# Optimization experiments

Hardware: AMD Instinct MI355X
Metric: run time of the kernel (lower is better)

## Reference

```python
import jax, jax.numpy as jnp
import numpy as np

N_NODES = 50000
N_EDGES = 800000
HID = 128
DEPTH = 10
N_GRAPHS = 512
IN_F = 32


def setup_inputs() -> dict:
    key = jax.random.key(0)
    ks = jax.random.split(key, 12)
    x = jax.random.normal(ks[0], (N_NODES, IN_F), jnp.float32)
    edge_index = jax.random.randint(ks[1], (2, N_EDGES), 0, N_NODES, dtype=jnp.int32)
    batch_map = jnp.sort(jax.random.randint(ks[2], (N_NODES,), 0, N_GRAPHS, dtype=jnp.int32))
    # parameters (PyG GraphConv: lin_rel has bias, lin_root has no bias)
    W_embed = jax.random.normal(ks[3], (IN_F, HID), jnp.float32) * 0.1
    W_rel = jax.random.normal(ks[4], (DEPTH, HID, HID), jnp.float32) * 0.05
    b_rel = jax.random.normal(ks[5], (DEPTH, HID), jnp.float32) * 0.01
    W_root = jax.random.normal(ks[6], (DEPTH, HID, HID), jnp.float32) * 0.05
    W_ws = jax.random.normal(ks[7], (DEPTH * HID, 1), jnp.float32) * 0.05
    b_ws = jax.random.normal(ks[8], (1,), jnp.float32) * 0.01
    W_sg = jax.random.normal(ks[9], (DEPTH * HID, IN_F), jnp.float32) * 0.05
    b_sg = jax.random.normal(ks[10], (IN_F,), jnp.float32) * 0.01
    return {
        "x": x, "edge_index": edge_index, "batch_map": batch_map,
        "num_graphs": N_GRAPHS,
        "W_embed": W_embed, "W_rel": W_rel, "b_rel": b_rel, "W_root": W_root,
        "W_ws": W_ws, "b_ws": b_ws, "W_sg": W_sg, "b_sg": b_sg,
    }


def reference(x, edge_index, batch_map, num_graphs,
              W_embed, W_rel, b_rel, W_root, W_ws, b_ws, W_sg, b_sg):
    n = x.shape[0]
    src, dst = edge_index[0], edge_index[1]
    h = x @ W_embed  # [N, 128]
    reps = []
    for i in range(DEPTH):
        # PyG GraphConv (aggr='add'): lin_rel(sum_j h_j) + lin_root(h_i)
        agg = jax.ops.segment_sum(h[src], dst, num_segments=n)  # [N, 128]
        h = agg @ W_rel[i] + b_rel[i] + h @ W_root[i]
        reps.append(h)
    out = jnp.concatenate(reps, axis=1)  # [N, 1280]
    # softmax over last dim of [N,1] logits (faithful: yields ones)
    sum_w = jax.nn.softmax(out @ W_ws + b_ws, axis=-1)  # [N, 1]
    out = sum_w * out
    pooled = jax.ops.segment_sum(out, batch_map, num_segments=num_graphs)  # [G, 1280]
    return pooled @ W_sg + b_sg  # [G, 32]
```

## Files before the change

### kernel.cpp

```cpp
#include <hip/hip_runtime.h>

#define N_NODES 50000
#define N_EDGES 800000
#define HID 128
#define DEPTH 10
#define N_GRAPHS 512
#define IN_F 32

#define BM 128
#define GBLK (50048 / BM)
#define PADN 50048

#define ROWW 256

#define SB 256
#define NSB ((N_NODES + SB - 1) / SB)

#define KSTEPS 24
#define PACK_CHUNKS (DEPTH * KSTEPS * 512)

typedef __attribute__((ext_vector_type(8))) short short8;
typedef __attribute__((ext_vector_type(4))) float f32x4;
typedef __attribute__((ext_vector_type(4))) unsigned uint4v;

__device__ __forceinline__ float bf2f(short u) {
    union { unsigned i; float f; } v; v.i = ((unsigned)(unsigned short)u) << 16; return v.f;
}
__device__ __forceinline__ short f2bf(float f) {
    union { float f; unsigned i; } v; v.f = f;
    unsigned r = (v.i + 0x7FFFu + ((v.i >> 16) & 1u)) >> 16;
    return (short)r;
}
__device__ __forceinline__ unsigned pack2(short lo, short hi) {
    return ((unsigned)(unsigned short)hi << 16) | (unsigned)(unsigned short)lo;
}

__global__ __launch_bounds__(256) void pack_weights(
    const float* __restrict__ Wrel, const float* __restrict__ Wroot,
    short* __restrict__ Bp) {
    int idx = blockIdx.x * 256 + threadIdx.x;
    if (idx >= PACK_CHUNKS) return;
    int layer = idx / (KSTEPS * 512);
    int rem = idx - layer * KSTEPS * 512;
    int ks = rem >> 9;
    int c = rem & 511;
    int kslot = c >> 7, n = c & 127;
    int term = ks >> 2;
    int kc = (ks & 3) * 32;
    const float* W = (term < 3 ? Wrel : Wroot) + (size_t)layer * HID * HID;
    bool lo = (term == 1 || term == 4);
    short out[8];
#pragma unroll
    for (int j = 0; j < 8; ++j) {
        int k = kc + kslot * 8 + j;
        float v = W[(size_t)k * HID + n];
        short hi = f2bf(v);
        if (lo) { v = v - bf2f(hi); hi = f2bf(v); }
        out[j] = hi;
    }
    *reinterpret_cast<short8*>(Bp + (size_t)idx * 8) = *reinterpret_cast<short8*>(out);
}

__global__ __launch_bounds__(128) void embed_kernel(
    const float* __restrict__ x, const float* __restrict__ W,
    short* __restrict__ hIL, short* __restrict__ hHr) {
    __shared__ float Ws[IN_F * HID];
    int t = threadIdx.x;
    for (int i = t; i < IN_F * HID; i += 128) Ws[i] = W[i];
    __syncthreads();
    int nbeg = blockIdx.x * 50;
    for (int n = nbeg; n < nbeg + 50; ++n) {
        float acc = 0.f;
#pragma unroll
        for (int k = 0; k < IN_F; ++k)
            acc += x[(size_t)n * IN_F + k] * Ws[k * HID + t];
        short hh = f2bf(acc);
        hIL[(size_t)n * ROWW + t] = hh;
        hIL[(size_t)n * ROWW + HID + t] = f2bf(acc - bf2f(hh));
        hHr[(size_t)n * HID + t] = hh;
    }
}

__global__ __launch_bounds__(256) void hist_kernel(const int* __restrict__ idx, int* __restrict__ count, int n) {
    int e = blockIdx.x * 256 + threadIdx.x;
    if (e < n) atomicAdd(&count[idx[e]], 1);
}

__global__ __launch_bounds__(SB) void scan_part1(
    const int* __restrict__ count, int* __restrict__ bsum, int n) {
    __shared__ int s[SB];
    int t = threadIdx.x;
    int i = blockIdx.x * SB + t;
    s[t] = (i < n) ? count[i] : 0;
    __syncthreads();
    for (int off = SB / 2; off >= 1; off >>= 1) {
        if (t < off) s[t] += s[t + off];
        __syncthreads();
    }
    if (t == 0) bsum[blockIdx.x] = s[0];
}

__global__ __launch_bounds__(256) void scan_part2(
    const int* __restrict__ bsum, int* __restrict__ boff, int nb) {
    __shared__ int s[256];
    int t = threadIdx.x;
    int v0 = (t < nb) ? bsum[t] : 0;
    s[t] = v0;
    __syncthreads();
    for (int off = 1; off < 256; off <<= 1) {
        int v = (t >= off) ? s[t - off] : 0;
        __syncthreads();
        s[t] += v;
        __syncthreads();
    }
    boff[t] = (t == 0) ? 0 : s[t - 1];
}

__global__ __launch_bounds__(SB) void scan_part3(
    const int* __restrict__ count, const int* __restrict__ boff,
    int* __restrict__ ptr, int* __restrict__ cursor, int n) {
    __shared__ int s[SB];
    int b = blockIdx.x, t = threadIdx.x;
    int i = b * SB + t;
    int v = (i < n) ? count[i] : 0;
    s[t] = v;
    __syncthreads();
    for (int off = 1; off < SB; off <<= 1) {
        int u = (t >= off) ? s[t - off] : 0;
        __syncthreads();
        s[t] += u;
        __syncthreads();
    }
    int excl = s[t] - v + boff[b];
    if (i < n) {
        ptr[i] = excl;
        cursor[i] = excl;
        if (i == n - 1) ptr[n] = excl + v;
    }
}

__global__ __launch_bounds__(256) void scatter_kernel(
    const int* __restrict__ src, const int* __restrict__ dst,
    int* __restrict__ cursor, int* __restrict__ sorted_src) {
    int e = blockIdx.x * 256 + threadIdx.x;
    if (e < N_EDGES) {
        int p = atomicAdd(&cursor[dst[e]], 1);
        sorted_src[p] = src[e];
    }
}

__global__ __launch_bounds__(256) void aggregate_kernel(
    const short* __restrict__ hHr, const int* __restrict__ row_ptr,
    const int* __restrict__ sorted_src, short* __restrict__ agg2) {
    int n = (blockIdx.x * 256 + threadIdx.x) >> 6;
    int lane = threadIdx.x & 63;
    const unsigned* __restrict__ R = (const unsigned*)hHr;
    int beg = row_ptr[n], end = row_ptr[n + 1];
    float a0 = 0.f, a1 = 0.f;
#define ACC(v) do { \
        union { unsigned u; float f; } u0, u1; \
        u0.u = (v) << 16; u1.u = (v) & 0xFFFF0000u; \
        a0 += u0.f; a1 += u1.f; } while (0)
    int j = beg;
    for (; j + 8 <= end; j += 8) {
        unsigned v[8];
#pragma unroll
        for (int u = 0; u < 8; ++u) {
            int s = __builtin_amdgcn_readfirstlane(sorted_src[j + u]);
            v[u] = R[(size_t)s * 64 + lane];
        }
#pragma unroll
        for (int u = 0; u < 8; ++u) ACC(v[u]);
    }
    for (; j + 2 <= end; j += 2) {
        int s0 = __builtin_amdgcn_readfirstlane(sorted_src[j]);
        int s1 = __builtin_amdgcn_readfirstlane(sorted_src[j + 1]);
        unsigned v0 = R[(size_t)s0 * 64 + lane];
        unsigned v1 = R[(size_t)s1 * 64 + lane];
        ACC(v0); ACC(v1);
    }
    if (j < end) {
        int s = __builtin_amdgcn_readfirstlane(sorted_src[j]);
        unsigned v = R[(size_t)s * 64 + lane];
        ACC(v);
    }
#undef ACC
    short h0 = f2bf(a0), h1 = f2bf(a1);
    unsigned hw = pack2(h0, h1);
    unsigned lw = pack2(f2bf(a0 - bf2f(h0)), f2bf(a1 - bf2f(h1)));
    ((unsigned*)agg2)[(size_t)n * 128 + lane] = hw;
    ((unsigned*)agg2)[(size_t)n * 128 + 64 + lane] = lw;
}

__global__ __launch_bounds__(512) void layer_gemm_mfma(
    const short* __restrict__ agg2, const short* __restrict__ hIL,
    const short* __restrict__ Bp, const float* __restrict__ bias,
    short* __restrict__ outIL, short* __restrict__ outH,
    const int* __restrict__ bmap, float* __restrict__ pooled, int layer,
    int write_h) {
    __shared__ __align__(16) char smem[34304];
    short* AbBuf = (short*)smem;
    short* BbBuf = (short*)(smem + 16384);
    float* Cs    = (float*)smem;
    int*   bmapS = (int*)(smem + 33792);

    int tid = threadIdx.x;
    int lane = tid & 63;
    int w = tid >> 6;
    int wr = w >> 2, wc = w & 3;
    int m0 = blockIdx.x * BM;

    int r0 = tid >> 2, q0 = tid & 3;

    f32x4 acc[4][2];
#pragma unroll
    for (int m = 0; m < 4; ++m)
#pragma unroll
        for (int n = 0; n < 2; ++n) acc[m][n] = (f32x4)0.f;

#define A_ADDR(src, row, f0, plane) \
    ((src) + (size_t)(row) * ROWW + (plane) * HID + (f0))

    {
        short8 a0 = *reinterpret_cast<const short8*>(A_ADDR(agg2, m0 + r0, q0 * 8, 0));
        short8 b0 = *reinterpret_cast<const short8*>(Bp + (size_t)tid * 8);
        *reinterpret_cast<short8*>(&AbBuf[(q0 * 128 + r0) * 8]) = a0;
        *reinterpret_cast<short8*>(&BbBuf[tid * 8]) = b0;
    }
    __syncthreads();

    int kb = lane >> 4;
    int rr = lane & 15;

    for (int ks = 0; ks < KSTEPS; ++ks) {
        int cur = ks & 1;
        short8 a0, b0;
        if (ks < KSTEPS - 1) {
            int nks = ks + 1;
            int term = nks >> 2;
            int kc = (nks & 3) * 32;
            const short* src2 = (term <= 2) ? agg2 : hIL;
            int plane = (term == 2 || term == 5) ? 1 : 0;
            a0 = *reinterpret_cast<const short8*>(A_ADDR(src2, m0 + r0, kc + q0 * 8, plane));
            b0 = *reinterpret_cast<const short8*>(Bp + (size_t)nks * 4096 + (size_t)tid * 8);
        }
        short8 af[4], bfr[2];
#pragma unroll
        for (int m = 0; m < 4; ++m)
            af[m] = *reinterpret_cast<const short8*>(&AbBuf[cur * 4096 + (kb * 128 + wr * 64 + m * 16 + rr) * 8]);
#pragma unroll
        for (int n = 0; n < 2; ++n)
            bfr[n] = *reinterpret_cast<const short8*>(&BbBuf[cur * 4096 + (kb * 128 + wc * 32 + n * 16 + rr) * 8]);
#pragma unroll
        for (int m = 0; m < 4; ++m)
#pragma unroll
            for (int n = 0; n < 2; ++n)
                acc[m][n] = __builtin_amdgcn_mfma_f32_16x16x32_bf16(af[m], bfr[n], acc[m][n], 0, 0, 0);
        if (ks < KSTEPS - 1) {
            int nb = cur ^ 1;
            *reinterpret_cast<short8*>(&AbBuf[nb * 4096 + (q0 * 128 + r0) * 8]) = a0;
            *reinterpret_cast<short8*>(&BbBuf[nb * 4096 + tid * 8]) = b0;
        }
        __syncthreads();
    }
#undef A_ADDR

    if (tid < 128) {
        int gi = m0 + tid;
        bmapS[tid] = bmap[gi < N_NODES ? gi : N_NODES - 1];
    }
    float bs[2];
    {
        int col = wc * 32 + rr;
#pragma unroll
        for (int n = 0; n < 2; ++n) bs[n] = bias[col + n * 16];
    }
    int colP = tid & 127;
    int quarter = tid >> 7;

    for (int c = 0; c < 2; ++c) {
        if (wr == c) {
            int colb = wc * 32 + rr;
#pragma unroll
            for (int m = 0; m < 4; ++m) {
#pragma unroll
                for (int n = 0; n < 2; ++n) {
#pragma unroll
                    for (int i = 0; i < 4; ++i) {
                        int lr = m * 16 + kb * 4 + i;
                        Cs[lr * 132 + colb + n * 16] = acc[m][n][i] + bs[n];
                    }
                }
            }
        }
        __syncthreads();

        if (write_h) {
#pragma unroll
            for (int pq = 0; pq < 2; ++pq) {
                int idx = pq * 512 + tid;
                int lr = idx >> 4;
                int oct = idx & 15;
                const float4* crow = reinterpret_cast<const float4*>(&Cs[lr * 132 + oct * 8]);
                float4 c0 = crow[0], c1 = crow[1];
                float v[8] = {c0.x, c0.y, c0.z, c0.w, c1.x, c1.y, c1.z, c1.w};
                unsigned hw[4], lw[4];
#pragma unroll
                for (int k = 0; k < 4; ++k) {
                    short ha = f2bf(v[2 * k]), hb = f2bf(v[2 * k + 1]);
                    short la = f2bf(v[2 * k] - bf2f(ha)), lb = f2bf(v[2 * k + 1] - bf2f(hb));
                    hw[k] = pack2(ha, hb);
                    lw[k] = pack2(la, lb);
                }
                int row = m0 + c * 64 + lr;
                unsigned* oI = (unsigned*)(outIL + (size_t)row * ROWW);
                unsigned* oH = (unsigned*)(outH + (size_t)row * HID);
                uint4v hv; hv.x = hw[0]; hv.y = hw[1]; hv.z = hw[2]; hv.w = hw[3];
                uint4v lv; lv.x = lw[0]; lv.y = lw[1]; lv.z = lw[2]; lv.w = lw[3];
                *reinterpret_cast<uint4v*>(oI + oct * 4) = hv;
                *reinterpret_cast<uint4v*>(oI + 64 + oct * 4) = lv;
                *reinterpret_cast<uint4v*>(oH + oct * 4) = hv;
            }
        }

        {
            float pacc = 0.f;
            int gprev = -1;
            float* pbase = pooled + (size_t)layer * HID + colP;
            for (int q = 0; q < 16; ++q) {
                int lr = quarter * 16 + q;
                int grow = m0 + c * 64 + lr;
                if (grow >= N_NODES) break;
                int g = bmapS[c * 64 + lr];
                float v = Cs[lr * 132 + colP];
                if (g != gprev) {
                    if (gprev >= 0) atomicAdd(pbase + (size_t)gprev * (DEPTH * HID), pacc);
                    gprev = g; pacc = v;
                } else {
                    pacc += v;
                }
            }
            if (gprev >= 0) atomicAdd(pbase + (size_t)gprev * (DEPTH * HID), pacc);
        }
        __syncthreads();
    }
}

__global__ __launch_bounds__(256) void final_kernel(
    const float* __restrict__ pooled, const float* __restrict__ Wsg,
    const float* __restrict__ bsg, float* __restrict__ out) {
    int t = threadIdx.x & 31;
    int g = blockIdx.x * 8 + (threadIdx.x >> 5);
    float acc = bsg[t];
    const float* prow = pooled + (size_t)g * (DEPTH * HID);
    for (int k = 0; k < DEPTH * HID; ++k)
        acc += prow[k] * Wsg[k * IN_F + t];
    out[g * IN_F + t] = acc;
}

extern "C" void kernel_launch(void* const* d_in, const int* in_sizes, int n_in,
                              void* d_out, int out_size, void* d_ws, size_t ws_size,
                              hipStream_t stream) {
    const float* x       = (const float*)d_in[0];
    const int*   edge    = (const int*)d_in[1];
    const int*   bmap    = (const int*)d_in[2];
    const float* W_embed = (const float*)d_in[4];
    const float* W_rel   = (const float*)d_in[5];
    const float* b_rel   = (const float*)d_in[6];
    const float* W_root  = (const float*)d_in[7];
    const float* W_sg    = (const float*)d_in[10];
    const float* b_sg    = (const float*)d_in[11];
    float* out = (float*)d_out;

    const int* src = edge;
    const int* dst = edge + N_EDGES;

    char* ws = (char*)d_ws;
    auto alloc = [&](size_t bytes) -> char* {
        char* p = ws;
        ws += (bytes + 255) & ~(size_t)255;
        return p;
    };
    const size_t rowB = (size_t)PADN * ROWW * 2;
    const size_t hB   = (size_t)PADN * HID * 2;
    short* h_a   = (short*)alloc(rowB);
    short* h_b   = (short*)alloc(rowB);
    short* hHr   = (short*)alloc(hB);
    short* agg2  = (short*)alloc(rowB);
    float* pooled = (float*)alloc((size_t)N_GRAPHS * DEPTH * HID * 4);
    int* counts     = (int*)alloc((size_t)N_NODES * 4);
    int* row_ptr    = (int*)alloc((size_t)(N_NODES + 1) * 4);
    int* cursor     = (int*)alloc((size_t)N_NODES * 4);
    int* sorted_src = (int*)alloc((size_t)N_EDGES * 4);
    int* bsum       = (int*)alloc((size_t)256 * 4);
    int* boff       = (int*)alloc((size_t)256 * 4);
    short* Bpacked  = (short*)alloc((size_t)PACK_CHUNKS * 8 * 2);

    hipMemsetAsync(counts, 0, (size_t)N_NODES * 4, stream);
    hipMemsetAsync(pooled, 0, (size_t)N_GRAPHS * DEPTH * HID * 4, stream);

    pack_weights<<<(PACK_CHUNKS + 255) / 256, 256, 0, stream>>>(W_rel, W_root, Bpacked);
    embed_kernel<<<1000, 128, 0, stream>>>(x, W_embed, h_a, hHr);

    hist_kernel<<<(N_EDGES + 255) / 256, 256, 0, stream>>>(dst, counts, N_EDGES);
    scan_part1<<<NSB, SB, 0, stream>>>(counts, bsum, N_NODES);
    scan_part2<<<1, 256, 0, stream>>>(bsum, boff, NSB);
    scan_part3<<<NSB, SB, 0, stream>>>(counts, boff, row_ptr, cursor, N_NODES);
    scatter_kernel<<<(N_EDGES + 255) / 256, 256, 0, stream>>>(src, dst, cursor, sorted_src);

    short *hc = h_a, *hn = h_b;
    for (int i = 0; i < DEPTH; ++i) {
        aggregate_kernel<<<(N_NODES + 3) / 4, 256, 0, stream>>>(hHr, row_ptr, sorted_src, agg2);
        layer_gemm_mfma<<<GBLK, 512, 0, stream>>>(agg2, hc,
                                                  Bpacked + (size_t)i * KSTEPS * 4096,
                                                  b_rel + (size_t)i * HID,
                                                  hn, hHr, bmap, pooled, i,
                                                  (i < DEPTH - 1) ? 1 : 0);
        short* t = hc; hc = hn; hn = t;
    }

    final_kernel<<<N_GRAPHS / 8, 256, 0, stream>>>(pooled, W_sg, b_sg, out);
}
```

Measured before the change: 802.7 us.

## Restructure GEMM k-loop to reuse A tiles; privatize histogram and bin CSR scatter

The layer GEMM now loads each A tile (agg hi/lo plane, h hi/lo plane) once and multiplies it by one or two packed B tiles (hi and lo weight splits), giving 16 A stages instead of 24. This cuts A-tile global loads and barriers per block. It costs more shared memory for a double-width B buffer. Separately, the edge histogram writes into 8 privatized count planes that are summed in the scan, and the CSR scatter bins destinations into 8 node ranges per edge chunk to reduce atomic contention and improve locality, at the cost of each edge being read 8 times.

New measurement: 716.1 us. -10.8%, faster.

```diff
diff --git a/kernel.cpp b/kernel.cpp
--- a/kernel.cpp
+++ b/kernel.cpp
@@ -16,8 +16,14 @@
 #define SB 256
 #define NSB ((N_NODES + SB - 1) / SB)
 
-#define KSTEPS 24
-#define PACK_CHUNKS (DEPTH * KSTEPS * 512)
+#define NBIN 8
+#define BINW ((N_NODES + NBIN - 1) / NBIN)
+#define NCH 125
+#define CHSZ (N_EDGES / NCH)
+
+#define NBT 24
+#define NAST 16
+#define PACK_CHUNKS (DEPTH * NBT * 512)
 
 typedef __attribute__((ext_vector_type(8))) short short8;
 typedef __attribute__((ext_vector_type(4))) float f32x4;
@@ -40,19 +46,22 @@
     short* __restrict__ Bp) {
     int idx = blockIdx.x * 256 + threadIdx.x;
     if (idx >= PACK_CHUNKS) return;
-    int layer = idx / (KSTEPS * 512);
-    int rem = idx - layer * KSTEPS * 512;
-    int ks = rem >> 9;
+    int layer = idx / (NBT * 512);
+    int rem = idx - layer * NBT * 512;
+    int t = rem >> 9;
     int c = rem & 511;
     int kslot = c >> 7, n = c & 127;
-    int term = ks >> 2;
-    int kc = (ks & 3) * 32;
-    const float* W = (term < 3 ? Wrel : Wroot) + (size_t)layer * HID * HID;
-    bool lo = (term == 1 || term == 4);
+    int kc, lo;
+    const float* W;
+    if (t < 8)       { kc = t >> 1;        W = Wrel;  lo = t & 1; }
+    else if (t < 12) { kc = t - 8;         W = Wrel;  lo = 0; }
+    else if (t < 20) { kc = (t - 12) >> 1; W = Wroot; lo = t & 1; }
+    else             { kc = t - 20;        W = Wroot; lo = 0; }
+    W += (size_t)layer * HID * HID;
     short out[8];
 #pragma unroll
     for (int j = 0; j < 8; ++j) {
-        int k = kc + kslot * 8 + j;
+        int k = kc * 32 + kslot * 8 + j;
         float v = W[(size_t)k * HID + n];
         short hi = f2bf(v);
         if (lo) { v = v - bf2f(hi); hi = f2bf(v); }
@@ -81,17 +90,26 @@
     }
 }
 
-__global__ __launch_bounds__(256) void hist_kernel(const int* __restrict__ idx, int* __restrict__ count, int n) {
+__global__ __launch_bounds__(256) void hist8_kernel(
+    const int* __restrict__ dst, int* __restrict__ counts8) {
     int e = blockIdx.x * 256 + threadIdx.x;
-    if (e < n) atomicAdd(&count[idx[e]], 1);
+    int plane = blockIdx.x & 7;
+    if (e < N_EDGES) atomicAdd(&counts8[(size_t)plane * N_NODES + dst[e]], 1);
 }
 
 __global__ __launch_bounds__(SB) void scan_part1(
-    const int* __restrict__ count, int* __restrict__ bsum, int n) {
+    const int* __restrict__ counts8, int* __restrict__ counts,
+    int* __restrict__ bsum, int n) {
     __shared__ int s[SB];
     int t = threadIdx.x;
     int i = blockIdx.x * SB + t;
-    s[t] = (i < n) ? count[i] : 0;
+    int v = 0;
+    if (i < n) {
+#pragma unroll
+        for (int p = 0; p < 8; ++p) v += counts8[(size_t)p * N_NODES + i];
+        counts[i] = v;
+    }
+    s[t] = v;
     __syncthreads();
     for (int off = SB / 2; off >= 1; off >>= 1) {
         if (t < off) s[t] += s[t + off];
@@ -139,13 +157,21 @@
     }
 }
 
-__global__ __launch_bounds__(256) void scatter_kernel(
+__global__ __launch_bounds__(256) void scatter8_kernel(
     const int* __restrict__ src, const int* __restrict__ dst,
     int* __restrict__ cursor, int* __restrict__ sorted_src) {
-    int e = blockIdx.x * 256 + threadIdx.x;
-    if (e < N_EDGES) {
-        int p = atomicAdd(&cursor[dst[e]], 1);
-        sorted_src[p] = src[e];
+    int s = blockIdx.x & 7;
+    int c = blockIdx.x >> 3;
+    int lo = s * BINW;
+    int hi = lo + BINW;
+    int base = c * CHSZ;
+    for (int e = base + threadIdx.x; e < base + CHSZ; e += 256) {
+        int d = dst[e];
+        int sv = src[e];
+        if (d >= lo && d < hi) {
+            int p = atomicAdd(&cursor[d], 1);
+            sorted_src[p] = sv;
+        }
     }
 }
 
@@ -198,11 +224,11 @@
     short* __restrict__ outIL, short* __restrict__ outH,
     const int* __restrict__ bmap, float* __restrict__ pooled, int layer,
     int write_h) {
-    __shared__ __align__(16) char smem[34304];
+    __shared__ __align__(16) char smem[49664];
     short* AbBuf = (short*)smem;
     short* BbBuf = (short*)(smem + 16384);
     float* Cs    = (float*)smem;
-    int*   bmapS = (int*)(smem + 33792);
+    int*   bmapS = (int*)(smem + 49152);
 
     int tid = threadIdx.x;
     int lane = tid & 63;
@@ -218,52 +244,73 @@
 #pragma unroll
         for (int n = 0; n < 2; ++n) acc[m][n] = (f32x4)0.f;
 
-#define A_ADDR(src, row, f0, plane) \
-    ((src) + (size_t)(row) * ROWW + (plane) * HID + (f0))
+#define NB_OF(a)   ((((a) >> 2) & 1) ? 1 : 2)
+#define BOFF_OF(a) (((a) < 4) ? (a) * 2 : ((a) < 8) ? 8 + ((a) - 4) \
+                    : ((a) < 12) ? 12 + ((a) - 8) * 2 : 20 + ((a) - 12))
+#define A_PTR(a) ((((a) >> 2) <= 1 ? agg2 : hIL) + ((((a) >> 2) & 1) ? HID : 0))
 
     {
-        short8 a0 = *reinterpret_cast<const short8*>(A_ADDR(agg2, m0 + r0, q0 * 8, 0));
+        const short* Ap = A_PTR(0);
+        short8 a0 = *reinterpret_cast<const short8*>(Ap + (size_t)(m0 + r0) * ROWW + q0 * 8);
         short8 b0 = *reinterpret_cast<const short8*>(Bp + (size_t)tid * 8);
+        short8 b1 = *reinterpret_cast<const short8*>(Bp + 4096 * 8 / 8 * 8 + (size_t)tid * 8 + 4096);
+        b1 = *reinterpret_cast<const short8*>(Bp + (size_t)4096 + (size_t)tid * 8);
         *reinterpret_cast<short8*>(&AbBuf[(q0 * 128 + r0) * 8]) = a0;
         *reinterpret_cast<short8*>(&BbBuf[tid * 8]) = b0;
+        *reinterpret_cast<short8*>(&BbBuf[4096 + tid * 8]) = b1;
     }
     __syncthreads();
 
     int kb = lane >> 4;
     int rr = lane & 15;
 
-    for (int ks = 0; ks < KSTEPS; ++ks) {
-        int cur = ks & 1;
-        short8 a0, b0;
-        if (ks < KSTEPS - 1) {
-            int nks = ks + 1;
-            int term = nks >> 2;
-            int kc = (nks & 3) * 32;
-            const short* src2 = (term <= 2) ? agg2 : hIL;
-            int plane = (term == 2 || term == 5) ? 1 : 0;
-            a0 = *reinterpret_cast<const short8*>(A_ADDR(src2, m0 + r0, kc + q0 * 8, plane));
-            b0 = *reinterpret_cast<const short8*>(Bp + (size_t)nks * 4096 + (size_t)tid * 8);
-        }
-        short8 af[4], bfr[2];
+    for (int a = 0; a < NAST; ++a) {
+        int cur = a & 1;
+        int nb = NB_OF(a);
+        short8 an, bn0, bn1;
+        int nbn = 0;
+        if (a < NAST - 1) {
+            int na = a + 1;
+            nbn = NB_OF(na);
+            int kc = (na & 3) * 32;
+            const short* Ap = A_PTR(na) + kc;
+            an = *reinterpret_cast<const short8*>(Ap + (size_t)(m0 + r0) * ROWW + q0 * 8);
+            const short* Bsrc = Bp + (size_t)BOFF_OF(na) * 4096;
+            bn0 = *reinterpret_cast<const short8*>(Bsrc + (size_t)tid * 8);
+            if (nbn == 2)
+                bn1 = *reinterpret_cast<const short8*>(Bsrc + (size_t)4096 + (size_t)tid * 8);
+        }
+        short8 af[4];
 #pragma unroll
         for (int m = 0; m < 4; ++m)
             af[m] = *reinterpret_cast<const short8*>(&AbBuf[cur * 4096 + (kb * 128 + wr * 64 + m * 16 + rr) * 8]);
 #pragma unroll
-        for (int n = 0; n < 2; ++n)
-            bfr[n] = *reinterpret_cast<const short8*>(&BbBuf[cur * 4096 + (kb * 128 + wc * 32 + n * 16 + rr) * 8]);
-#pragma unroll
-        for (int m = 0; m < 4; ++m)
-#pragma unroll
-            for (int n = 0; n < 2; ++n)
-                acc[m][n] = __builtin_amdgcn_mfma_f32_16x16x32_bf16(af[m], bfr[n], acc[m][n], 0, 0, 0);
-        if (ks < KSTEPS - 1) {
-            int nb = cur ^ 1;
-            *reinterpret_cast<short8*>(&AbBuf[nb * 4096 + (q0 * 128 + r0) * 8]) = a0;
-            *reinterpret_cast<short8*>(&BbBuf[nb * 4096 + tid * 8]) = b0;
-        }
-        __syncthreads();
-    }
-#undef A_ADDR
+        for (int j = 0; j < 2; ++j) {
+            if (j < nb) {
+                short8 bfr[2];
+#pragma unroll
+                for (int n = 0; n < 2; ++n)
+                    bfr[n] = *reinterpret_cast<const short8*>(
+                        &BbBuf[cur * 8192 + j * 4096 + (kb * 128 + wc * 32 + n * 16 + rr) * 8]);
+#pragma unroll
+                for (int m = 0; m < 4; ++m)
+#pragma unroll
+                    for (int n = 0; n < 2; ++n)
+                        acc[m][n] = __builtin_amdgcn_mfma_f32_16x16x32_bf16(af[m], bfr[n], acc[m][n], 0, 0, 0);
+            }
+        }
+        if (a < NAST - 1) {
+            int nxt = cur ^ 1;
+            *reinterpret_cast<short8*>(&AbBuf[nxt * 4096 + (q0 * 128 + r0) * 8]) = an;
+            *reinterpret_cast<short8*>(&BbBuf[nxt * 8192 + tid * 8]) = bn0;
+            if (nbn == 2)
+                *reinterpret_cast<short8*>(&BbBuf[nxt * 8192 + 4096 + tid * 8]) = bn1;
+        }
+        __syncthreads();
+    }
+#undef NB_OF
+#undef BOFF_OF
+#undef A_PTR
 
     if (tid < 128) {
         int gi = m0 + tid;
@@ -388,6 +435,7 @@
     short* hHr   = (short*)alloc(hB);
     short* agg2  = (short*)alloc(rowB);
     float* pooled = (float*)alloc((size_t)N_GRAPHS * DEPTH * HID * 4);
+    int* counts8    = (int*)alloc((size_t)8 * N_NODES * 4);
     int* counts     = (int*)alloc((size_t)N_NODES * 4);
     int* row_ptr    = (int*)alloc((size_t)(N_NODES + 1) * 4);
     int* cursor     = (int*)alloc((size_t)N_NODES * 4);
@@ -396,23 +444,23 @@
     int* boff       = (int*)alloc((size_t)256 * 4);
     short* Bpacked  = (short*)alloc((size_t)PACK_CHUNKS * 8 * 2);
 
-    hipMemsetAsync(counts, 0, (size_t)N_NODES * 4, stream);
+    hipMemsetAsync(counts8, 0, (size_t)8 * N_NODES * 4, stream);
     hipMemsetAsync(pooled, 0, (size_t)N_GRAPHS * DEPTH * HID * 4, stream);
 
     pack_weights<<<(PACK_CHUNKS + 255) / 256, 256, 0, stream>>>(W_rel, W_root, Bpacked);
     embed_kernel<<<1000, 128, 0, stream>>>(x, W_embed, h_a, hHr);
 
-    hist_kernel<<<(N_EDGES + 255) / 256, 256, 0, stream>>>(dst, counts, N_EDGES);
-    scan_part1<<<NSB, SB, 0, stream>>>(counts, bsum, N_NODES);
+    hist8_kernel<<<(N_EDGES + 255) / 256, 256, 0, stream>>>(dst, counts8);
+    scan_part1<<<NSB, SB, 0, stream>>>(counts8, counts, bsum, N_NODES);
     scan_part2<<<1, 256, 0, stream>>>(bsum, boff, NSB);
     scan_part3<<<NSB, SB, 0, stream>>>(counts, boff, row_ptr, cursor, N_NODES);
-    scatter_kernel<<<(N_EDGES + 255) / 256, 256, 0, stream>>>(src, dst, cursor, sorted_src);
+    scatter8_kernel<<<NBIN * NCH, 256, 0, stream>>>(src, dst, cursor, sorted_src);
 
     short *hc = h_a, *hn = h_b;
     for (int i = 0; i < DEPTH; ++i) {
         aggregate_kernel<<<(N_NODES + 3) / 4, 256, 0, stream>>>(hHr, row_ptr, sorted_src, agg2);
         layer_gemm_mfma<<<GBLK, 512, 0, stream>>>(agg2, hc,
-                                                  Bpacked + (size_t)i * KSTEPS * 4096,
+                                                  Bpacked + (size_t)i * NBT * 4096,
                                                   b_rel + (size_t)i * HID,
                                                   hn, hHr, bmap, pooled, i,
                                                   (i < DEPTH - 1) ? 1 : 0);
```
